# Kernel optimization log

Measured on AMD Instinct MI355X. Metric: run time of the kernel, lower is better.

## Reference

```python
import jax, jax.numpy as jnp
import numpy as np

B, IN, OUT = 4096, 512, 512
NUM_KNOTS, DEGREE = 10, 3


def setup_inputs() -> dict:
    key = jax.random.key(0)
    k1, k2 = jax.random.split(key)
    x = jax.random.normal(k1, (B, IN), dtype=jnp.float32)
    # coefficients of all out*in edge splines: [out, in, num_knots-1, degree+1]
    coeff = jax.random.normal(k2, (OUT, IN, NUM_KNOTS - 1, DEGREE + 1), dtype=jnp.float32) * 0.1
    scale = jnp.ones((OUT,), dtype=jnp.float32)
    return {"x": x, "coeff": coeff, "scale": scale}


def reference(x, coeff, scale):
    # x: [B, IN]; coeff: [OUT, IN, S, P]; scale: [OUT]
    out_f, in_f, S, P = coeff.shape
    K = S + 1
    knots = jnp.linspace(-1.0, 1.0, K)            # shared uniform knots
    xc = jnp.clip(x, -1.0, 1.0)
    seg = jnp.clip(jnp.searchsorted(knots[1:], xc), 0, S - 1)  # [B, IN]
    lo = knots[seg]
    t = (xc - lo) / (knots[seg + 1] - lo)          # [B, IN]
    tpow = t[..., None] ** jnp.arange(P, dtype=x.dtype)        # [B, IN, P]
    onehot = jax.nn.one_hot(seg, S, dtype=x.dtype)             # [B, IN, S]
    # A[b,i,s,p] = onehot * t^p ; contraction with coeff is a single GEMM
    A = onehot[..., :, None] * tpow[..., None, :]              # [B, IN, S, P]
    y = jnp.einsum('bisp,jisp->bj', A, coeff)                  # [B, OUT]
    return y * scale
```

## Files before the change

kernel.cpp:

```cpp
#include <hip/hip_runtime.h>

#define B_DIM   4096
#define IN_DIM  512
#define OUT_DIM 512
#define KTOT    18432
#define BK      64
#define KSPLIT  8
#define KPER    2304
#define NT      36

using f32x4 = __attribute__((ext_vector_type(4))) float;
using s16x8 = __attribute__((ext_vector_type(8))) short;
using u32x4 = __attribute__((ext_vector_type(4))) unsigned int;

__device__ __forceinline__ unsigned int f2bf(float f) {
    unsigned int u = __float_as_uint(f);
    return (u + 0x7FFFu + ((u >> 16) & 1u)) >> 16;
}

__device__ __forceinline__ void glds16(const void* g, void* l) {
    __builtin_amdgcn_global_load_lds(
        (const __attribute__((address_space(1))) unsigned int*)g,
        (__attribute__((address_space(3))) unsigned int*)l,
        16, 0, 0);
}

__device__ __forceinline__ uint2 spline_rec_packed(float xv) {
    float xc = fminf(fmaxf(xv, -1.0f), 1.0f);
    double xd = (double)xc;
    int s = 0;
#pragma unroll
    for (int k = 1; k <= 8; ++k)
        s += ((-1.0 + (double)k * (2.0 / 9.0)) < xd) ? 1 : 0;
    double lo = -1.0 + (double)s * (2.0 / 9.0);
    double hi = -1.0 + (double)(s + 1) * (2.0 / 9.0);
    float t  = (float)((xd - lo) / (hi - lo));
    float t2 = t * t, t3 = t2 * t;
    uint2 r;
    r.x = f2bf(t)  | (f2bf(t2) << 16);
    r.y = f2bf(t3) | ((unsigned int)s << 16);
    return r;
}

__global__ void prep_x_kernel(const float* __restrict__ x, uint2* __restrict__ tp) {
    int idx = blockIdx.x * 256 + threadIdx.x;
    if (idx >= B_DIM * IN_DIM) return;
    tp[idx] = spline_rec_packed(x[idx]);
}

__global__ void prep_coeff2(const float* __restrict__ c,
                            const float* __restrict__ scale,
                            u32x4* __restrict__ cbf2) {
    int g = blockIdx.x * 256 + threadIdx.x;
    if (g >= (OUT_DIM * KTOT) / 8) return;
    int row = g & 127;
    int oct = (g >> 7) & 7;
    int hi  = g >> 10;
    int ntg = hi / 288;
    int kt  = hi - ntg * 288;
    int j = ntg * 128 + row;
    int k = kt * 64 + oct * 8;
    float s = scale[j];
    const float* src = c + (size_t)j * KTOT + k;
    f32x4 a = *(const f32x4*)src;
    f32x4 b = *(const f32x4*)(src + 4);
    u32x4 o;
    o.x = f2bf(a.x * s) | (f2bf(a.y * s) << 16);
    o.y = f2bf(a.z * s) | (f2bf(a.w * s) << 16);
    o.z = f2bf(b.x * s) | (f2bf(b.y * s) << 16);
    o.w = f2bf(b.z * s) | (f2bf(b.w * s) << 16);
    cbf2[g] = o;
}

__device__ __forceinline__ void scat3(char* Aq, int ar, int ah,
                                      uint2 q0, uint2 q1, uint2 q2,
                                      int ifirst, int k0) {
#pragma unroll
    for (int cc = 0; cc < 3; ++cc) {
        uint2 rec = cc == 0 ? q0 : (cc == 1 ? q1 : q2);
        int i = ifirst + cc;
        if (i < IN_DIM) {
            int s = (int)(rec.y >> 16);
            int off = i * 36 + s * 4 - k0;
            if (off >= 0 && off < 64 && ((off >> 5) == ah)) {
                uint2 w;
                w.x = 0x3F80u | (rec.x << 16);
                w.y = (rec.x >> 16) | (rec.y << 16);
                *(uint2*)(Aq + (off >> 3) * 2048 + ar * 16 + (off & 4) * 2) = w;
            }
        }
    }
}

__launch_bounds__(256, 2)
__global__ void kan_gemm_db(const unsigned short* __restrict__ cbf2,
                            const uint2* __restrict__ tp,
                            float* __restrict__ out) {
    __shared__ u32x4 ldsRaw[65536 / 16];
    char* lds = (char*)ldsRaw;

    const int tid  = threadIdx.x;
    const int lane = tid & 63;
    const int wave = tid >> 6;
    const int wm = wave >> 1, wn = wave & 1;
    const int l15 = lane & 15, lhi = lane >> 4;

    const int bid = blockIdx.x;
    const int nt = bid & 3;
    const int ks = (bid >> 2) & 7;
    const int mt = bid >> 5;
    const int m0g = mt * 128, n0g = nt * 128;
    const int kbase = ks * KPER;

    const int ar = tid & 127, ah = tid >> 7;

    const uint2* tpRow = tp + (size_t)(m0g + ar) * IN_DIM;
    const char*  cbase = (const char*)cbf2 + (size_t)(nt * 288 + ks * NT) * 16384;

    f32x4 acc[4][4] = {};
    uint2 r0, r1, r2;

    {
        char* A0 = lds;
        char* B0 = lds + 32768;
        const int if0 = kbase / 36;
        uint2 q0 = tpRow[if0];
        uint2 q1 = tpRow[if0 + 1 < IN_DIM ? if0 + 1 : IN_DIM - 1];
        uint2 q2 = tpRow[if0 + 2 < IN_DIM ? if0 + 2 : IN_DIM - 1];
        u32x4 z = {};
#pragma unroll
        for (int zi = 0; zi < 4; ++zi)
            *(u32x4*)(A0 + (ah * 4 + zi) * 2048 + ar * 16) = z;
        scat3(A0, ar, ah, q0, q1, q2, if0, kbase);
#pragma unroll
        for (int it = 0; it < 4; ++it)
            glds16(cbase + it * 4096 + tid * 16, B0 + it * 4096 + tid * 16);
        const int if1 = (kbase + BK) / 36;
        r0 = tpRow[if1];
        r1 = tpRow[if1 + 1 < IN_DIM ? if1 + 1 : IN_DIM - 1];
        r2 = tpRow[if1 + 2 < IN_DIM ? if1 + 2 : IN_DIM - 1];
        __syncthreads();
    }

    for (int t = 0; t < NT; ++t) {
        const int p = t & 1;
        const char* Ap = lds + p * 16384;
        const char* Bp = lds + 32768 + p * 16384;
        char* Aq = lds + (p ^ 1) * 16384;
        char* Bq = lds + 32768 + (p ^ 1) * 16384;

        if (t + 1 < NT) {
            const int k0n = kbase + (t + 1) * BK;
            u32x4 z = {};
#pragma unroll
            for (int zi = 0; zi < 4; ++zi)
                *(u32x4*)(Aq + (ah * 4 + zi) * 2048 + ar * 16) = z;
            scat3(Aq, ar, ah, r0, r1, r2, k0n / 36, k0n);
            const char* srcT = cbase + (size_t)(t + 1) * 16384;
#pragma unroll
            for (int it = 0; it < 4; ++it)
                glds16(srcT + it * 4096 + tid * 16, Bq + it * 4096 + tid * 16);
            const int tn = t + 2 < NT ? t + 2 : NT - 1;
            const int ifn = (kbase + tn * BK) / 36;
            r0 = tpRow[ifn];
            r1 = tpRow[ifn + 1 < IN_DIM ? ifn + 1 : IN_DIM - 1];
            r2 = tpRow[ifn + 2 < IN_DIM ? ifn + 2 : IN_DIM - 1];
        }

#pragma unroll
        for (int kh = 0; kh < 2; ++kh) {
            s16x8 a[4], b[4];
#pragma unroll
            for (int mf = 0; mf < 4; ++mf)
                a[mf] = *(const s16x8*)(Ap + (kh * 4 + lhi) * 2048 + (wm * 64 + mf * 16 + l15) * 16);
#pragma unroll
            for (int nf = 0; nf < 4; ++nf)
                b[nf] = *(const s16x8*)(Bp + (kh * 4 + lhi) * 2048 + (wn * 64 + nf * 16 + l15) * 16);
#pragma unroll
            for (int mf = 0; mf < 4; ++mf)
#pragma unroll
                for (int nf = 0; nf < 4; ++nf)
                    acc[mf][nf] = __builtin_amdgcn_mfma_f32_16x16x32_bf16(a[mf], b[nf], acc[mf][nf], 0, 0, 0);
        }

        __syncthreads();
    }

#pragma unroll
    for (int mf = 0; mf < 4; ++mf) {
        const int rg = m0g + wm * 64 + mf * 16 + lhi * 4;
#pragma unroll
        for (int nf = 0; nf < 4; ++nf) {
            const int cg = n0g + wn * 64 + nf * 16 + l15;
#pragma unroll
            for (int e = 0; e < 4; ++e)
                atomicAdd(out + (size_t)(rg + e) * OUT_DIM + cg, acc[mf][nf][e]);
        }
    }
}

#define BM 128
#define BN 128
#define FKPER  4608
#define FSTEPS 72
__launch_bounds__(256, 2)
__global__ void kan_gemm_ref(const float* __restrict__ x,
                             const float* __restrict__ coeff,
                             const float* __restrict__ scale,
                             float* __restrict__ out) {
    __shared__ unsigned short AsF[BM * 72];
    __shared__ unsigned short BsF[8 * BN * 8];
    const int tid  = threadIdx.x;
    const int lane = tid & 63;
    const int wave = tid >> 6;
    const int wm = wave >> 1, wn = wave & 1;
    const int l15 = lane & 15, lhi = lane >> 4;
    const int bid = blockIdx.x;
    const int nt = bid & 3;
    const int ks = (bid >> 2) & 3;
    const int mt = bid >> 4;
    const int m0g = mt * BM, n0g = nt * BN, kbase = ks * FKPER;
    const int ar = tid >> 1, ah = tid & 1;
    const int abrow = m0g + ar;
    const int bjg = n0g + (tid & 127);
    const float bscale = scale[bjg];
    char* AsB = (char*)AsF;
    char* BsB = (char*)BsF;
    f32x4 acc[4][4] = {};
    for (int step = 0; step < FSTEPS; ++step) {
        const int k0 = kbase + step * BK;
        {
            char* rb = AsB + ar * 144;
            u32x4 z = {};
            if (ah == 0) {
#pragma unroll
                for (int z4 = 0; z4 < 4; ++z4) *(u32x4*)(rb + z4 * 16) = z;
            } else {
#pragma unroll
                for (int z4 = 4; z4 < 9; ++z4) *(u32x4*)(rb + z4 * 16) = z;
            }
            const int ifirst = k0 / 36;
#pragma unroll
            for (int ii = 0; ii < 2; ++ii) {
                const int cand = ah + ii * 2;
                const int i = ifirst + cand;
                if (cand < 3 && i * 36 < k0 + BK && i < IN_DIM) {
                    uint2 rec = spline_rec_packed(x[(size_t)abrow * IN_DIM + i]);
                    int s = (int)(rec.y >> 16);
                    const int off = i * 36 + s * 4 - k0;
                    unsigned int w0 = 0x3F80u | (rec.x << 16);
                    unsigned int w1 = (rec.x >> 16) | (rec.y << 16);
                    if (off >= 0 && off <= 62) *(unsigned int*)(rb + off * 2) = w0;
                    const int off2 = off + 2;
                    if (off2 >= 0 && off2 <= 62) *(unsigned int*)(rb + off2 * 2) = w1;
                }
            }
        }
#pragma unroll
        for (int it = 0; it < 4; ++it) {
            const int q  = it * 256 + tid;
            const int c  = q >> 7;
            const int kk = k0 + c * 8;
            f32x4 a = *(const f32x4*)(coeff + (size_t)bjg * KTOT + kk);
            f32x4 b = *(const f32x4*)(coeff + (size_t)bjg * KTOT + kk + 4);
            u32x4 o;
            o.x = f2bf(a.x * bscale) | (f2bf(a.y * bscale) << 16);
            o.y = f2bf(a.z * bscale) | (f2bf(a.w * bscale) << 16);
            o.z = f2bf(b.x * bscale) | (f2bf(b.y * bscale) << 16);
            o.w = f2bf(b.z * bscale) | (f2bf(b.w * bscale) << 16);
            *(u32x4*)(BsB + q * 16) = o;
        }
        __syncthreads();
#pragma unroll
        for (int kh = 0; kh < 2; ++kh) {
            const int kk = kh * 32;
            s16x8 a[4], b[4];
#pragma unroll
            for (int mf = 0; mf < 4; ++mf)
                a[mf] = *(const s16x8*)(AsB + (wm * 64 + mf * 16 + l15) * 144 + (kk + lhi * 8) * 2);
#pragma unroll
            for (int nf = 0; nf < 4; ++nf)
                b[nf] = *(const s16x8*)(BsB + (kh * 4 + lhi) * 2048 + (wn * 64 + nf * 16 + l15) * 16);
#pragma unroll
            for (int mf = 0; mf < 4; ++mf)
#pragma unroll
                for (int nf = 0; nf < 4; ++nf)
                    acc[mf][nf] = __builtin_amdgcn_mfma_f32_16x16x32_bf16(a[mf], b[nf], acc[mf][nf], 0, 0, 0);
        }
        __syncthreads();
    }
#pragma unroll
    for (int mf = 0; mf < 4; ++mf) {
        const int cmBase = m0g + wm * 64 + mf * 16 + lhi * 4;
#pragma unroll
        for (int nf = 0; nf < 4; ++nf) {
            const int cn = n0g + wn * 64 + nf * 16 + l15;
#pragma unroll
            for (int e = 0; e < 4; ++e)
                atomicAdd(out + (size_t)(cmBase + e) * OUT_DIM + cn, acc[mf][nf][e]);
        }
    }
}

extern "C" void kernel_launch(void* const* d_in, const int* in_sizes, int n_in,
                              void* d_out, int out_size, void* d_ws, size_t ws_size,
                              hipStream_t stream) {
    const float* x     = (const float*)d_in[0];
    const float* coeff = (const float*)d_in[1];
    const float* scale = (const float*)d_in[2];
    float* out = (float*)d_out;

    const size_t SZ_CBF = (size_t)OUT_DIM * KTOT * 2;
    const size_t SZ_TP  = (size_t)B_DIM * IN_DIM * 8;
    const size_t NEED   = SZ_CBF + SZ_TP;

    hipMemsetAsync(d_out, 0, (size_t)B_DIM * OUT_DIM * sizeof(float), stream);

    if (ws_size >= NEED) {
        unsigned short* cbf2 = (unsigned short*)d_ws;
        uint2*          tp   = (uint2*)((char*)d_ws + SZ_CBF);
        prep_coeff2<<<4608, 256, 0, stream>>>(coeff, scale, (u32x4*)cbf2);
        prep_x_kernel<<<8192, 256, 0, stream>>>(x, tp);
        kan_gemm_db<<<1024, 256, 0, stream>>>(cbf2, tp, out);
    } else {
        kan_gemm_ref<<<512, 256, 0, stream>>>(x, coeff, scale, out);
    }
}
```

Baseline: 176.0 us.

## Replace 128x128 GEMM with 256x256 eight-wave tile and phased barrier schedule

The main GEMM moves from 128x128 tiles with 4 waves and 1024 blocks to 256x256 tiles with 8 waves, 512 threads and 256 blocks. The coefficient pre-pack layout changes to match, and LDS doubles to 128KB. Each k-step is split into four phases that interleave LDS fragment loads, A-tile zeroing, the global-to-LDS copy of B, and MFMA bursts. The phases use explicit barriers, waitcnt and setprio. The aim is more data reuse per LDS byte, fewer atomic adds, and better overlap of loads with MFMAs, at the cost of only 256 blocks (about one per CU), which limits occupancy and latency hiding.

Result: faster. 172.3 us (-2.1%).

```diff
diff --git a/kernel.cpp b/kernel.cpp
--- a/kernel.cpp
+++ b/kernel.cpp
@@ -7,7 +7,7 @@
 #define BK      64
 #define KSPLIT  8
 #define KPER    2304
-#define NT      36
+#define NT8     36
 
 using f32x4 = __attribute__((ext_vector_type(4))) float;
 using s16x8 = __attribute__((ext_vector_type(8))) short;
@@ -53,12 +53,12 @@
                             u32x4* __restrict__ cbf2) {
     int g = blockIdx.x * 256 + threadIdx.x;
     if (g >= (OUT_DIM * KTOT) / 8) return;
-    int row = g & 127;
-    int oct = (g >> 7) & 7;
-    int hi  = g >> 10;
-    int ntg = hi / 288;
+    int row = g & 255;
+    int oct = (g >> 8) & 7;
+    int hi  = g >> 11;
+    int ntg = hi >= 288 ? 1 : 0;
     int kt  = hi - ntg * 288;
-    int j = ntg * 128 + row;
+    int j = ntg * 256 + row;
     int k = kt * 64 + oct * 8;
     float s = scale[j];
     const float* src = c + (size_t)j * KTOT + k;
@@ -86,109 +86,136 @@
                 uint2 w;
                 w.x = 0x3F80u | (rec.x << 16);
                 w.y = (rec.x >> 16) | (rec.y << 16);
-                *(uint2*)(Aq + (off >> 3) * 2048 + ar * 16 + (off & 4) * 2) = w;
+                *(uint2*)(Aq + (off >> 3) * 4096 + ar * 16 + (off & 4) * 2) = w;
             }
         }
     }
 }
 
-__launch_bounds__(256, 2)
-__global__ void kan_gemm_db(const unsigned short* __restrict__ cbf2,
-                            const uint2* __restrict__ tp,
-                            float* __restrict__ out) {
-    __shared__ u32x4 ldsRaw[65536 / 16];
+#define BAR()   __builtin_amdgcn_s_barrier()
+#define SB0()   __builtin_amdgcn_sched_barrier(0)
+#define WLGKM() asm volatile("s_waitcnt lgkmcnt(0)" ::: "memory")
+#define WVM0()  asm volatile("s_waitcnt vmcnt(0)"   ::: "memory")
+
+__launch_bounds__(512, 2)
+__global__ void kan_gemm8(const unsigned short* __restrict__ cbf2,
+                          const uint2* __restrict__ tp,
+                          float* __restrict__ out) {
+    __shared__ u32x4 ldsRaw[131072 / 16];
     char* lds = (char*)ldsRaw;
 
     const int tid  = threadIdx.x;
     const int lane = tid & 63;
     const int wave = tid >> 6;
-    const int wm = wave >> 1, wn = wave & 1;
+    const int wm = wave >> 2, wn = wave & 3;
     const int l15 = lane & 15, lhi = lane >> 4;
 
     const int bid = blockIdx.x;
-    const int nt = bid & 3;
-    const int ks = (bid >> 2) & 7;
-    const int mt = bid >> 5;
-    const int m0g = mt * 128, n0g = nt * 128;
+    const int ks = bid >> 5;
+    const int mt = (bid >> 1) & 15;
+    const int nt = bid & 1;
+    const int m0g = mt * 256, n0g = nt * 256;
     const int kbase = ks * KPER;
 
-    const int ar = tid & 127, ah = tid >> 7;
+    const int ar = tid & 255, ah = tid >> 8;
 
     const uint2* tpRow = tp + (size_t)(m0g + ar) * IN_DIM;
-    const char*  cbase = (const char*)cbf2 + (size_t)(nt * 288 + ks * NT) * 16384;
-
-    f32x4 acc[4][4] = {};
+    const char*  cbase = (const char*)cbf2 + (size_t)(nt * 288 + ks * NT8) * 32768;
+
+    const int aoff = (wm * 128 + l15) * 16;
+    const int boff = (wn * 64  + l15) * 16;
+    const int ohi  = lhi * 4096;
+
+    f32x4 acc[8][4] = {};
+    s16x8 av[4], bv[4];
     uint2 r0, r1, r2;
 
     {
         char* A0 = lds;
-        char* B0 = lds + 32768;
+        char* B0 = lds + 65536;
         const int if0 = kbase / 36;
-        uint2 q0 = tpRow[if0];
-        uint2 q1 = tpRow[if0 + 1 < IN_DIM ? if0 + 1 : IN_DIM - 1];
-        uint2 q2 = tpRow[if0 + 2 < IN_DIM ? if0 + 2 : IN_DIM - 1];
+        r0 = tpRow[if0];
+        r1 = tpRow[if0 + 1 < IN_DIM ? if0 + 1 : IN_DIM - 1];
+        r2 = tpRow[if0 + 2 < IN_DIM ? if0 + 2 : IN_DIM - 1];
         u32x4 z = {};
 #pragma unroll
         for (int zi = 0; zi < 4; ++zi)
-            *(u32x4*)(A0 + (ah * 4 + zi) * 2048 + ar * 16) = z;
-        scat3(A0, ar, ah, q0, q1, q2, if0, kbase);
+            *(u32x4*)(A0 + (ah * 4 + zi) * 4096 + ar * 16) = z;
+        scat3(A0, ar, ah, r0, r1, r2, if0, kbase);
 #pragma unroll
         for (int it = 0; it < 4; ++it)
-            glds16(cbase + it * 4096 + tid * 16, B0 + it * 4096 + tid * 16);
+            glds16(cbase + it * 8192 + tid * 16, B0 + it * 8192 + tid * 16);
+        WVM0();
         const int if1 = (kbase + BK) / 36;
         r0 = tpRow[if1];
         r1 = tpRow[if1 + 1 < IN_DIM ? if1 + 1 : IN_DIM - 1];
         r2 = tpRow[if1 + 2 < IN_DIM ? if1 + 2 : IN_DIM - 1];
-        __syncthreads();
-    }
-
-    for (int t = 0; t < NT; ++t) {
+        WLGKM();
+        BAR();
+        SB0();
+    }
+
+#define LOAD_A(KH, MH)                                                          \
+    _Pragma("unroll") for (int c_ = 0; c_ < 4; ++c_)                            \
+        av[c_] = *(const s16x8*)(Ap + (KH) * 16384 + ohi + aoff + ((MH) * 4 + c_) * 256);
+#define LOAD_B(KH)                                                              \
+    _Pragma("unroll") for (int c_ = 0; c_ < 4; ++c_)                            \
+        bv[c_] = *(const s16x8*)(Bp + (KH) * 16384 + ohi + boff + c_ * 256);
+#define MFMA_Q(MH)                                                              \
+    _Pragma("unroll") for (int mf_ = 0; mf_ < 4; ++mf_)                         \
+        _Pragma("unroll") for (int nf_ = 0; nf_ < 4; ++nf_)                     \
+            acc[(MH) * 4 + mf_][nf_] = __builtin_amdgcn_mfma_f32_16x16x32_bf16( \
+                av[mf_], bv[nf_], acc[(MH) * 4 + mf_][nf_], 0, 0, 0);
+#define PHASE_MID() BAR(); WLGKM(); SB0(); __builtin_amdgcn_s_setprio(1)
+#define PHASE_END() __builtin_amdgcn_s_setprio(0); BAR(); SB0()
+
+    for (int t = 0; t < NT8; ++t) {
         const int p = t & 1;
-        const char* Ap = lds + p * 16384;
-        const char* Bp = lds + 32768 + p * 16384;
-        char* Aq = lds + (p ^ 1) * 16384;
-        char* Bq = lds + 32768 + (p ^ 1) * 16384;
-
-        if (t + 1 < NT) {
-            const int k0n = kbase + (t + 1) * BK;
-            u32x4 z = {};
-#pragma unroll
-            for (int zi = 0; zi < 4; ++zi)
-                *(u32x4*)(Aq + (ah * 4 + zi) * 2048 + ar * 16) = z;
-            scat3(Aq, ar, ah, r0, r1, r2, k0n / 36, k0n);
-            const char* srcT = cbase + (size_t)(t + 1) * 16384;
-#pragma unroll
-            for (int it = 0; it < 4; ++it)
-                glds16(srcT + it * 4096 + tid * 16, Bq + it * 4096 + tid * 16);
-            const int tn = t + 2 < NT ? t + 2 : NT - 1;
-            const int ifn = (kbase + tn * BK) / 36;
-            r0 = tpRow[ifn];
-            r1 = tpRow[ifn + 1 < IN_DIM ? ifn + 1 : IN_DIM - 1];
-            r2 = tpRow[ifn + 2 < IN_DIM ? ifn + 2 : IN_DIM - 1];
-        }
-
-#pragma unroll
-        for (int kh = 0; kh < 2; ++kh) {
-            s16x8 a[4], b[4];
-#pragma unroll
-            for (int mf = 0; mf < 4; ++mf)
-                a[mf] = *(const s16x8*)(Ap + (kh * 4 + lhi) * 2048 + (wm * 64 + mf * 16 + l15) * 16);
-#pragma unroll
-            for (int nf = 0; nf < 4; ++nf)
-                b[nf] = *(const s16x8*)(Bp + (kh * 4 + lhi) * 2048 + (wn * 64 + nf * 16 + l15) * 16);
-#pragma unroll
-            for (int mf = 0; mf < 4; ++mf)
-#pragma unroll
-                for (int nf = 0; nf < 4; ++nf)
-                    acc[mf][nf] = __builtin_amdgcn_mfma_f32_16x16x32_bf16(a[mf], b[nf], acc[mf][nf], 0, 0, 0);
-        }
-
-        __syncthreads();
-    }
-
-#pragma unroll
-    for (int mf = 0; mf < 4; ++mf) {
-        const int rg = m0g + wm * 64 + mf * 16 + lhi * 4;
+        const char* Ap = lds + p * 32768;
+        const char* Bp = lds + 65536 + p * 32768;
+        char* Aq = lds + (p ^ 1) * 32768;
+        char* Bq = lds + 65536 + (p ^ 1) * 32768;
+        const int tt1 = t + 1 < NT8 ? t + 1 : NT8 - 1;
+        const int k0n = kbase + tt1 * BK;
+        const char* srcT = cbase + (size_t)tt1 * 32768;
+        u32x4 z = {};
+
+        LOAD_B(0); LOAD_A(0, 0);
+        *(u32x4*)(Aq + (ah * 4 + 0) * 4096 + ar * 16) = z;
+        glds16(srcT + 0 * 8192 + tid * 16, Bq + 0 * 8192 + tid * 16);
+        PHASE_MID(); MFMA_Q(0); PHASE_END();
+
+        LOAD_A(0, 1);
+        *(u32x4*)(Aq + (ah * 4 + 1) * 4096 + ar * 16) = z;
+        glds16(srcT + 1 * 8192 + tid * 16, Bq + 1 * 8192 + tid * 16);
+        PHASE_MID(); MFMA_Q(1); PHASE_END();
+
+        LOAD_B(1); LOAD_A(1, 0);
+        *(u32x4*)(Aq + (ah * 4 + 2) * 4096 + ar * 16) = z;
+        glds16(srcT + 2 * 8192 + tid * 16, Bq + 2 * 8192 + tid * 16);
+        PHASE_MID(); MFMA_Q(0); PHASE_END();
+
+        LOAD_A(1, 1);
+        *(u32x4*)(Aq + (ah * 4 + 3) * 4096 + ar * 16) = z;
+        {
+            const int if1 = k0n / 36;
+            scat3(Aq, ar, ah, r0, r1, r2, if1, k0n);
+        }
+        glds16(srcT + 3 * 8192 + tid * 16, Bq + 3 * 8192 + tid * 16);
+        WVM0();
+        {
+            const int tt2 = t + 2 < NT8 ? t + 2 : NT8 - 1;
+            const int if2 = (kbase + tt2 * BK) / 36;
+            r0 = tpRow[if2];
+            r1 = tpRow[if2 + 1 < IN_DIM ? if2 + 1 : IN_DIM - 1];
+            r2 = tpRow[if2 + 2 < IN_DIM ? if2 + 2 : IN_DIM - 1];
+        }
+        PHASE_MID(); MFMA_Q(1); PHASE_END();
+    }
+
+#pragma unroll
+    for (int mf = 0; mf < 8; ++mf) {
+        const int rg = m0g + wm * 128 + mf * 16 + lhi * 4;
 #pragma unroll
         for (int nf = 0; nf < 4; ++nf) {
             const int cg = n0g + wn * 64 + nf * 16 + l15;
@@ -201,6 +228,7 @@
 
 #define BM 128
 #define BN 128
+#define FBK 64
 #define FKPER  4608
 #define FSTEPS 72
 __launch_bounds__(256, 2)
@@ -228,7 +256,7 @@
     char* BsB = (char*)BsF;
     f32x4 acc[4][4] = {};
     for (int step = 0; step < FSTEPS; ++step) {
-        const int k0 = kbase + step * BK;
+        const int k0 = kbase + step * FBK;
         {
             char* rb = AsB + ar * 144;
             u32x4 z = {};
@@ -244,7 +272,7 @@
             for (int ii = 0; ii < 2; ++ii) {
                 const int cand = ah + ii * 2;
                 const int i = ifirst + cand;
-                if (cand < 3 && i * 36 < k0 + BK && i < IN_DIM) {
+                if (cand < 3 && i * 36 < k0 + FBK && i < IN_DIM) {
                     uint2 rec = spline_rec_packed(x[(size_t)abrow * IN_DIM + i]);
                     int s = (int)(rec.y >> 16);
                     const int off = i * 36 + s * 4 - k0;
@@ -321,7 +349,7 @@
         uint2*          tp   = (uint2*)((char*)d_ws + SZ_CBF);
         prep_coeff2<<<4608, 256, 0, stream>>>(coeff, scale, (u32x4*)cbf2);
         prep_x_kernel<<<8192, 256, 0, stream>>>(x, tp);
-        kan_gemm_db<<<1024, 256, 0, stream>>>(cbf2, tp, out);
+        kan_gemm8<<<256, 512, 0, stream>>>(cbf2, tp, out);
     } else {
         kan_gemm_ref<<<512, 256, 0, stream>>>(x, coeff, scale, out);
     }
```
